# Performance work log

Hardware: AMD Instinct MI355X
Metric: run time of the kernel (lower is better)

The kernel has to match this reference:

```python
import jax, jax.numpy as jnp
import numpy as np

N_NODES = 100000
N_EDGES = 1600000
NIN = 128
NHID = 128
N_GRAPHS = 1024


def _gcn_conv(x, src, dst, norm, W, b, n_nodes):
    """PyG-style GCNConv: linear (no bias) -> normalized scatter-add -> + bias."""
    xw = x @ W                                   # [N, out]
    msg = xw[src] * norm[:, None]                # gather + edge-normalize, [E', out]
    out = jax.ops.segment_sum(msg, dst, num_segments=n_nodes)
    return out + b


def _gcn_norm(edge_index, n_nodes):
    """Add self-loops and compute symmetric deg^{-1/2} normalization per edge."""
    loops = jnp.arange(n_nodes, dtype=edge_index.dtype)
    src = jnp.concatenate([edge_index[0], loops])
    dst = jnp.concatenate([edge_index[1], loops])
    deg = jax.ops.segment_sum(jnp.ones_like(dst, dtype=jnp.float32), dst,
                              num_segments=n_nodes)
    deg_isqrt = jnp.where(deg > 0, jax.lax.rsqrt(jnp.maximum(deg, 1.0)), 0.0)
    norm = deg_isqrt[src] * deg_isqrt[dst]
    return src, dst, norm


def setup_inputs() -> dict:
    key = jax.random.key(0)
    ks = jax.random.split(key, 8)
    x = jax.random.normal(ks[0], (N_NODES, NIN), dtype=jnp.float32)
    edge_index = jax.random.randint(ks[1], (2, N_EDGES), 0, N_NODES, dtype=jnp.int64)
    batch = jnp.sort(jax.random.randint(ks[2], (N_NODES,), 0, N_GRAPHS, dtype=jnp.int64))
    s_in = 1.0 / np.sqrt(NIN)
    s_h = 1.0 / np.sqrt(NHID)
    return {
        "x": x,
        "edge_index": edge_index,
        "batch": batch,
        "W1": jax.random.normal(ks[3], (NIN, NHID), dtype=jnp.float32) * s_in,
        "b1": jnp.zeros((NHID,), dtype=jnp.float32),
        "W2": jax.random.normal(ks[4], (NHID, NHID), dtype=jnp.float32) * s_h,
        "b2": jnp.zeros((NHID,), dtype=jnp.float32),
        "W3": jax.random.normal(ks[5], (NHID, NHID), dtype=jnp.float32) * s_h,
        "b3": jnp.zeros((NHID,), dtype=jnp.float32),
        "Wfc": jax.random.normal(ks[6], (NHID, 1), dtype=jnp.float32) * s_h,
        "bfc": jnp.zeros((1,), dtype=jnp.float32),
    }


def reference(x, edge_index, batch, W1, b1, W2, b2, W3, b3, Wfc, bfc):
    n_nodes = x.shape[0]
    src, dst, norm = _gcn_norm(edge_index, n_nodes)
    h = jax.nn.relu(_gcn_conv(x, src, dst, norm, W1, b1, n_nodes))
    h = jax.nn.relu(_gcn_conv(h, src, dst, norm, W2, b2, n_nodes))
    h = jax.nn.relu(_gcn_conv(h, src, dst, norm, W3, b3, n_nodes))
    # global mean pool over graphs in the batch
    sums = jax.ops.segment_sum(h, batch, num_segments=N_GRAPHS)      # [G, NHID]
    cnts = jax.ops.segment_sum(jnp.ones((n_nodes,), dtype=h.dtype), batch,
                               num_segments=N_GRAPHS)
    pooled = sums / jnp.maximum(cnts, 1.0)[:, None]
    return pooled @ Wfc + bfc                                        # [G, 1]
```

## Files before the change

### kernel.cpp

```cpp
#include <hip/hip_runtime.h>

#define N_NODES   100000
#define N_EDGES   1600000
#define NFEAT     128
#define N_GRAPHS  1024

#define BSHIFT  6
#define NBUCK   1563
#define NSUB    8
#define SUBCAP  256
#define CURSTRIDE 16

typedef unsigned int uint32;
typedef unsigned short ushort;
typedef __attribute__((ext_vector_type(8))) short short8;
typedef __attribute__((ext_vector_type(4))) float f32x4;

__device__ inline ushort f2b(float f) {
    uint32 x = __float_as_uint(f);
    uint32 r = x + 0x7fffu + ((x >> 16) & 1u);
    return (ushort)(r >> 16);
}
__device__ inline float blo(uint32 u) { return __uint_as_float(u << 16); }
__device__ inline float bhi(uint32 u) { return __uint_as_float(u & 0xffff0000u); }

__global__ __launch_bounds__(256) void k_scatter(const int* __restrict__ src, const int* __restrict__ dst,
                                                 int* __restrict__ cur, uint32* __restrict__ bbuf) {
    int e = blockIdx.x * 256 + threadIdx.x;
    int sub = blockIdx.x & (NSUB - 1);
    if (e < N_EDGES) {
        int s = src[e], d = dst[e];
        int b = d >> BSHIFT;
        int slot = (b << 3) | sub;
        int p = atomicAdd(&cur[slot * CURSTRIDE], 1);
        if (p < SUBCAP)
            bbuf[slot * SUBCAP + p] = (uint32)(((d & 63) << 17) | s);
    }
}

__global__ __launch_bounds__(256) void k_bucketscan(const int* __restrict__ cur, int* __restrict__ bucketBase,
                                                    int* __restrict__ offsets) {
    __shared__ int wsum[4];
    int t = threadIdx.x;
    int v[7];
    int ts = 0;
    #pragma unroll
    for (int i = 0; i < 7; ++i) {
        int b = t * 7 + i;
        int sz = 0;
        if (b < NBUCK) {
            #pragma unroll
            for (int s = 0; s < NSUB; ++s) {
                int c = cur[((b << 3) | s) * CURSTRIDE];
                sz += (c < SUBCAP) ? c : SUBCAP;
            }
        }
        v[i] = sz;
        ts += sz;
    }
    int lane = t & 63, w = t >> 6;
    int inc = ts;
    #pragma unroll
    for (int d = 1; d < 64; d <<= 1) {
        int u = __shfl_up(inc, d, 64);
        if (lane >= d) inc += u;
    }
    if (lane == 63) wsum[w] = inc;
    __syncthreads();
    int wpre = 0;
    for (int i = 0; i < w; ++i) wpre += wsum[i];
    int run = wpre + inc - ts;
    #pragma unroll
    for (int i = 0; i < 7; ++i) {
        int b = t * 7 + i;
        if (b < NBUCK) bucketBase[b] = run;
        run += v[i];
    }
    if (t == 255) offsets[N_NODES] = run;
}

__global__ __launch_bounds__(256) void k_build(const uint32* __restrict__ bbuf, const int* __restrict__ cur,
                                               const int* __restrict__ bucketBase, int* __restrict__ col,
                                               int* __restrict__ offsets, float* __restrict__ dinv) {
    int b = blockIdx.x;
    __shared__ uint32 ebuf[NSUB * SUBCAP];
    __shared__ int sorted[NSUB * SUBCAP];
    __shared__ int hist[64], lcur[64];
    __shared__ int subOff[NSUB + 1];
    int t = threadIdx.x;
    if (t == 0) {
        int run = 0;
        #pragma unroll
        for (int s = 0; s < NSUB; ++s) {
            subOff[s] = run;
            int c = cur[((b << 3) | s) * CURSTRIDE];
            run += (c < SUBCAP) ? c : SUBCAP;
        }
        subOff[NSUB] = run;
    }
    if (t < 64) hist[t] = 0;
    __syncthreads();
    int cnt = subOff[NSUB];
    #pragma unroll
    for (int s = 0; s < NSUB; ++s) {
        int n = subOff[s + 1] - subOff[s];
        const uint32* p = bbuf + ((b << 3) | s) * SUBCAP;
        for (int i = t; i < n; i += 256) ebuf[subOff[s] + i] = p[i];
    }
    __syncthreads();
    for (int i = t; i < cnt; i += 256) atomicAdd(&hist[ebuf[i] >> 17], 1);
    __syncthreads();
    int nb = b << BSHIFT;
    if (t < 64) {
        int c = hist[t];
        int inc = c;
        #pragma unroll
        for (int d = 1; d < 64; d <<= 1) {
            int u = __shfl_up(inc, d, 64);
            if (t >= d) inc += u;
        }
        int excl = inc - c;
        lcur[t] = excl;
        int node = nb + t;
        if (node < N_NODES) {
            offsets[node] = bucketBase[b] + excl;
            dinv[node] = rsqrtf((float)(c + 1));
        }
    }
    __syncthreads();
    for (int i = t; i < cnt; i += 256) {
        uint32 p = ebuf[i];
        int lp = atomicAdd(&lcur[p >> 17], 1);
        sorted[lp] = (int)(p & 0x1FFFF);
    }
    __syncthreads();
    int base = bucketBase[b];
    for (int i = t; i < cnt; i += 256) col[base + i] = sorted[i];
}

__global__ __launch_bounds__(256) void k_castw(const float* __restrict__ W1, const float* __restrict__ W2,
                                               const float* __restrict__ W3, ushort* __restrict__ WT) {
    int i = blockIdx.x * blockDim.x + threadIdx.x;
    if (i >= 3 * NFEAT * NFEAT) return;
    int l = i >> 14;
    int j = i & 16383;
    int n = j >> 7;
    int k = j & 127;
    const float* W = (l == 0) ? W1 : (l == 1) ? W2 : W3;
    WT[i] = f2b(W[k * NFEAT + n]);
}

#define WT_STRIDE 136
#define GEMM_EPILOGUE \
    __syncthreads(); \
    { \
        ushort* sC = sWT; \
        int colBase = lane & 15; \
        _Pragma("unroll") \
        for (int r = 0; r < 4; ++r) { \
            int lr = wave * 16 + kg * 4 + r; \
            _Pragma("unroll") \
            for (int nt = 0; nt < 8; ++nt) \
                sC[lr * NFEAT + nt * 16 + colBase] = f2b(acc[nt][r]); \
        } \
    } \
    __syncthreads(); \
    { \
        int rowBase = blockIdx.x * 64; \
        const float4* sC4 = (const float4*)sWT; \
        for (int i = t; i < 1024; i += 256) { \
            int row = i >> 4; \
            int gr = rowBase + row; \
            if (gr < M) ((float4*)(C + (size_t)gr * NFEAT))[i & 15] = sC4[i]; \
        } \
    }

__global__ __launch_bounds__(256) void k_gemm(const ushort* __restrict__ A,
                                              const ushort* __restrict__ WTl,
                                              ushort* __restrict__ C, int M) {
    __shared__ ushort sWT[NFEAT * WT_STRIDE];
    int t = threadIdx.x;
    for (int i = t; i < NFEAT * 16; i += 256) {
        int n = i >> 4, c = i & 15;
        *(float4*)(sWT + n * WT_STRIDE + c * 8) = ((const float4*)WTl)[i];
    }
    int wave = t >> 6, lane = t & 63;
    int m0 = blockIdx.x * 64 + wave * 16;
    int mRow = m0 + (lane & 15);
    if (mRow >= M) mRow = M - 1;
    int kg = lane >> 4;
    const short8* Ap = (const short8*)(A + (size_t)mRow * NFEAT + kg * 8);
    short8 a0 = Ap[0];
    short8 a1 = Ap[4];
    short8 a2 = Ap[8];
    short8 a3 = Ap[12];
    __syncthreads();

    f32x4 acc[8];
    #pragma unroll
    for (int nt = 0; nt < 8; ++nt) acc[nt] = (f32x4){0.f, 0.f, 0.f, 0.f};

    #pragma unroll
    for (int nt = 0; nt < 8; ++nt) {
        int n = nt * 16 + (lane & 15);
        const short8* Bp = (const short8*)(sWT + n * WT_STRIDE + kg * 8);
        short8 b0 = Bp[0];
        short8 b1 = Bp[4];
        short8 b2 = Bp[8];
        short8 b3 = Bp[12];
        acc[nt] = __builtin_amdgcn_mfma_f32_16x16x32_bf16(a0, b0, acc[nt], 0, 0, 0);
        acc[nt] = __builtin_amdgcn_mfma_f32_16x16x32_bf16(a1, b1, acc[nt], 0, 0, 0);
        acc[nt] = __builtin_amdgcn_mfma_f32_16x16x32_bf16(a2, b2, acc[nt], 0, 0, 0);
        acc[nt] = __builtin_amdgcn_mfma_f32_16x16x32_bf16(a3, b3, acc[nt], 0, 0, 0);
    }
    GEMM_EPILOGUE
}

__device__ inline short8 cvt8(const float* p) {
    float4 v0 = ((const float4*)p)[0];
    float4 v1 = ((const float4*)p)[1];
    short8 r;
    r[0] = (short)f2b(v0.x); r[1] = (short)f2b(v0.y);
    r[2] = (short)f2b(v0.z); r[3] = (short)f2b(v0.w);
    r[4] = (short)f2b(v1.x); r[5] = (short)f2b(v1.y);
    r[6] = (short)f2b(v1.z); r[7] = (short)f2b(v1.w);
    return r;
}

__global__ __launch_bounds__(256) void k_gemm_x(const float* __restrict__ A,
                                                const ushort* __restrict__ WTl,
                                                ushort* __restrict__ C, int M) {
    __shared__ ushort sWT[NFEAT * WT_STRIDE];
    int t = threadIdx.x;
    for (int i = t; i < NFEAT * 16; i += 256) {
        int n = i >> 4, c = i & 15;
        *(float4*)(sWT + n * WT_STRIDE + c * 8) = ((const float4*)WTl)[i];
    }
    int wave = t >> 6, lane = t & 63;
    int m0 = blockIdx.x * 64 + wave * 16;
    int mRow = m0 + (lane & 15);
    if (mRow >= M) mRow = M - 1;
    int kg = lane >> 4;
    const float* Ap = A + (size_t)mRow * NFEAT + kg * 8;
    short8 a0 = cvt8(Ap);
    short8 a1 = cvt8(Ap + 32);
    short8 a2 = cvt8(Ap + 64);
    short8 a3 = cvt8(Ap + 96);
    __syncthreads();

    f32x4 acc[8];
    #pragma unroll
    for (int nt = 0; nt < 8; ++nt) acc[nt] = (f32x4){0.f, 0.f, 0.f, 0.f};

    #pragma unroll
    for (int nt = 0; nt < 8; ++nt) {
        int n = nt * 16 + (lane & 15);
        const short8* Bp = (const short8*)(sWT + n * WT_STRIDE + kg * 8);
        short8 b0 = Bp[0];
        short8 b1 = Bp[4];
        short8 b2 = Bp[8];
        short8 b3 = Bp[12];
        acc[nt] = __builtin_amdgcn_mfma_f32_16x16x32_bf16(a0, b0, acc[nt], 0, 0, 0);
        acc[nt] = __builtin_amdgcn_mfma_f32_16x16x32_bf16(a1, b1, acc[nt], 0, 0, 0);
        acc[nt] = __builtin_amdgcn_mfma_f32_16x16x32_bf16(a2, b2, acc[nt], 0, 0, 0);
        acc[nt] = __builtin_amdgcn_mfma_f32_16x16x32_bf16(a3, b3, acc[nt], 0, 0, 0);
    }
    GEMM_EPILOGUE
}

#define AGG_BODY4 \
    float dn = dinv[n]; \
    int half = lane >> 4; \
    int fl = lane & 15; \
    const uint4* XW4 = (const uint4*)XWu; \
    uint4 sv = XW4[(size_t)n * 16 + fl]; \
    float ws = (half == 0) ? dn * dn : 0.f; \
    float a0 = ws * blo(sv.x), a1 = ws * bhi(sv.x); \
    float a2 = ws * blo(sv.y), a3 = ws * bhi(sv.y); \
    float a4 = ws * blo(sv.z), a5 = ws * bhi(sv.z); \
    float a6 = ws * blo(sv.w), a7 = ws * bhi(sv.w); \
    int e0 = off[n], e1 = off[n + 1]; \
    for (int base = e0; base < e1; base += 64) { \
        int len = e1 - base; if (len > 64) len = 64; \
        int cm = (lane < len) ? col[base + lane] : 0; \
        float wm = (lane < len) ? dn * dinv[cm] : 0.f; \
        int j = 0; \
        for (; j + 16 <= len; j += 16) { \
            uint4 u[4]; float w[4]; \
            _Pragma("unroll") \
            for (int p = 0; p < 4; ++p) { \
                int idx = j + 4 * p + half; \
                int cc = __shfl(cm, idx, 64); \
                w[p] = __shfl(wm, idx, 64); \
                u[p] = XW4[(size_t)cc * 16 + fl]; \
            } \
            _Pragma("unroll") \
            for (int p = 0; p < 4; ++p) { \
                a0 = fmaf(w[p], blo(u[p].x), a0); a1 = fmaf(w[p], bhi(u[p].x), a1); \
                a2 = fmaf(w[p], blo(u[p].y), a2); a3 = fmaf(w[p], bhi(u[p].y), a3); \
                a4 = fmaf(w[p], blo(u[p].z), a4); a5 = fmaf(w[p], bhi(u[p].z), a5); \
                a6 = fmaf(w[p], blo(u[p].w), a6); a7 = fmaf(w[p], bhi(u[p].w), a7); \
            } \
        } \
        for (; j < len; j += 4) { \
            int rem = len - j; \
            int idx = j + ((half < rem) ? half : 0); \
            int cc = __shfl(cm, idx, 64); \
            float ww = __shfl(wm, idx, 64); \
            if (half >= rem) ww = 0.f; \
            uint4 u = XW4[(size_t)cc * 16 + fl]; \
            a0 = fmaf(ww, blo(u.x), a0); a1 = fmaf(ww, bhi(u.x), a1); \
            a2 = fmaf(ww, blo(u.y), a2); a3 = fmaf(ww, bhi(u.y), a3); \
            a4 = fmaf(ww, blo(u.z), a4); a5 = fmaf(ww, bhi(u.z), a5); \
            a6 = fmaf(ww, blo(u.w), a6); a7 = fmaf(ww, bhi(u.w), a7); \
        } \
    } \
    a0 += __shfl_xor(a0, 32, 64); a0 += __shfl_xor(a0, 16, 64); \
    a1 += __shfl_xor(a1, 32, 64); a1 += __shfl_xor(a1, 16, 64); \
    a2 += __shfl_xor(a2, 32, 64); a2 += __shfl_xor(a2, 16, 64); \
    a3 += __shfl_xor(a3, 32, 64); a3 += __shfl_xor(a3, 16, 64); \
    a4 += __shfl_xor(a4, 32, 64); a4 += __shfl_xor(a4, 16, 64); \
    a5 += __shfl_xor(a5, 32, 64); a5 += __shfl_xor(a5, 16, 64); \
    a6 += __shfl_xor(a6, 32, 64); a6 += __shfl_xor(a6, 16, 64); \
    a7 += __shfl_xor(a7, 32, 64); a7 += __shfl_xor(a7, 16, 64);

__global__ __launch_bounds__(256) void k_agg(const uint32* __restrict__ XWu, const int* __restrict__ col,
                                             const int* __restrict__ off, const float* __restrict__ dinv,
                                             const float* __restrict__ bias, uint32* __restrict__ Hu) {
    int wid = (blockIdx.x * blockDim.x + threadIdx.x) >> 6;
    int lane = threadIdx.x & 63;
    if (wid >= N_NODES) return;
    int n = wid;
    AGG_BODY4
    if (half == 0) {
        float4 bb0 = ((const float4*)bias)[2 * fl];
        float4 bb1 = ((const float4*)bias)[2 * fl + 1];
        float r0 = fmaxf(a0 + bb0.x, 0.f), r1 = fmaxf(a1 + bb0.y, 0.f);
        float r2 = fmaxf(a2 + bb0.z, 0.f), r3 = fmaxf(a3 + bb0.w, 0.f);
        float r4 = fmaxf(a4 + bb1.x, 0.f), r5 = fmaxf(a5 + bb1.y, 0.f);
        float r6 = fmaxf(a6 + bb1.z, 0.f), r7 = fmaxf(a7 + bb1.w, 0.f);
        uint4 o;
        o.x = (uint32)f2b(r0) | ((uint32)f2b(r1) << 16);
        o.y = (uint32)f2b(r2) | ((uint32)f2b(r3) << 16);
        o.z = (uint32)f2b(r4) | ((uint32)f2b(r5) << 16);
        o.w = (uint32)f2b(r6) | ((uint32)f2b(r7) << 16);
        ((uint4*)Hu)[(size_t)n * 16 + fl] = o;
    }
}

__global__ __launch_bounds__(256) void k_agg_fc(const uint32* __restrict__ XWu, const int* __restrict__ col,
                                                const int* __restrict__ off, const float* __restrict__ dinv,
                                                const float* __restrict__ bias, const float* __restrict__ Wfc,
                                                float* __restrict__ nodeS) {
    int wid = (blockIdx.x * blockDim.x + threadIdx.x) >> 6;
    int lane = threadIdx.x & 63;
    if (wid >= N_NODES) return;
    int n = wid;
    AGG_BODY4
    float4 bb0 = ((const float4*)bias)[2 * fl];
    float4 bb1 = ((const float4*)bias)[2 * fl + 1];
    float4 wf0 = ((const float4*)Wfc)[2 * fl];
    float4 wf1 = ((const float4*)Wfc)[2 * fl + 1];
    float s = fmaxf(a0 + bb0.x, 0.f) * wf0.x + fmaxf(a1 + bb0.y, 0.f) * wf0.y
            + fmaxf(a2 + bb0.z, 0.f) * wf0.z + fmaxf(a3 + bb0.w, 0.f) * wf0.w
            + fmaxf(a4 + bb1.x, 0.f) * wf1.x + fmaxf(a5 + bb1.y, 0.f) * wf1.y
            + fmaxf(a6 + bb1.z, 0.f) * wf1.z + fmaxf(a7 + bb1.w, 0.f) * wf1.w;
    s += __shfl_xor(s, 8, 64);
    s += __shfl_xor(s, 4, 64);
    s += __shfl_xor(s, 2, 64);
    s += __shfl_xor(s, 1, 64);
    if (lane == 0) nodeS[n] = s;
}

__device__ inline int lower_bound_dev(const int* a, int n, int key) {
    int lo = 0, hi = n;
    while (lo < hi) {
        int mid = (lo + hi) >> 1;
        if (a[mid] < key) lo = mid + 1; else hi = mid;
    }
    return lo;
}

__global__ __launch_bounds__(256) void k_pool(const float* __restrict__ nodeS, const int* __restrict__ batch,
                                              const float* __restrict__ bfc, float* __restrict__ out) {
    int g = blockIdx.x;
    int t = threadIdx.x;
    int lo = lower_bound_dev(batch, N_NODES, g);
    int hi = lower_bound_dev(batch, N_NODES, g + 1);
    float s = 0.f;
    for (int i = lo + t; i < hi; i += 256) s += nodeS[i];
    for (int d = 32; d > 0; d >>= 1) s += __shfl_down(s, d, 64);
    __shared__ float ws[4];
    int lane = t & 63, w = t >> 6;
    if (lane == 0) ws[w] = s;
    __syncthreads();
    if (t == 0) {
        float tot = ws[0] + ws[1] + ws[2] + ws[3];
        float cnt = (float)(hi - lo);
        out[g] = tot / fmaxf(cnt, 1.0f) + bfc[0];
    }
}

extern "C" void kernel_launch(void* const* d_in, const int* in_sizes, int n_in,
                              void* d_out, int out_size, void* d_ws, size_t ws_size,
                              hipStream_t stream) {
    const float* x    = (const float*)d_in[0];
    const int*   ei   = (const int*)d_in[1];
    const int*   batch= (const int*)d_in[2];
    const float* W1   = (const float*)d_in[3];
    const float* b1   = (const float*)d_in[4];
    const float* W2   = (const float*)d_in[5];
    const float* b2   = (const float*)d_in[6];
    const float* W3   = (const float*)d_in[7];
    const float* b3   = (const float*)d_in[8];
    const float* Wfc  = (const float*)d_in[9];
    const float* bfc  = (const float*)d_in[10];
    float* out = (float*)d_out;

    const int* src = ei;
    const int* dst = ei + N_EDGES;

    char* p = (char*)d_ws;
    auto carve = [&](size_t bytes) { void* r = (void*)p; p += (bytes + 255) & ~(size_t)255; return r; };
    int*    cur       = (int*)   carve(sizeof(int) * (size_t)NBUCK * NSUB * CURSTRIDE);
    uint32* bbuf      = (uint32*)carve(sizeof(uint32) * (size_t)NBUCK * NSUB * SUBCAP);
    int*    bucketBase= (int*)   carve(sizeof(int) * (NBUCK + 1));
    float*  dinv      = (float*) carve(sizeof(float) * N_NODES);
    int*    offsets   = (int*)   carve(sizeof(int) * (N_NODES + 1));
    int*    col       = (int*)   carve(sizeof(int) * N_EDGES);
    ushort* XW        = (ushort*)carve(sizeof(short) * (size_t)N_NODES * NFEAT);
    ushort* H         = (ushort*)carve(sizeof(short) * (size_t)N_NODES * NFEAT);
    ushort* WT        = (ushort*)carve(sizeof(short) * 3 * NFEAT * NFEAT);
    float*  nodeS     = (float*) carve(sizeof(float) * N_NODES);

    const int edgeBlocks = (N_EDGES + 255) / 256;
    const int waveNodeBlocks = (N_NODES * 64 + 255) / 256;
    const int gemmBlocks = (N_NODES + 63) / 64;

    hipMemsetAsync(cur, 0, sizeof(int) * (size_t)NBUCK * NSUB * CURSTRIDE, stream);
    k_scatter<<<edgeBlocks, 256, 0, stream>>>(src, dst, cur, bbuf);
    k_bucketscan<<<1, 256, 0, stream>>>(cur, bucketBase, offsets);
    k_build<<<NBUCK, 256, 0, stream>>>(bbuf, cur, bucketBase, col, offsets, dinv);

    k_castw<<<(3 * NFEAT * NFEAT + 255) / 256, 256, 0, stream>>>(W1, W2, W3, WT);

    k_gemm_x<<<gemmBlocks, 256, 0, stream>>>(x, WT, XW, N_NODES);
    k_agg<<<waveNodeBlocks, 256, 0, stream>>>((const uint32*)XW, col, offsets, dinv, b1, (uint32*)H);
    k_gemm<<<gemmBlocks, 256, 0, stream>>>(H, WT + NFEAT * NFEAT, XW, N_NODES);
    k_agg<<<waveNodeBlocks, 256, 0, stream>>>((const uint32*)XW, col, offsets, dinv, b2, (uint32*)H);
    k_gemm<<<gemmBlocks, 256, 0, stream>>>(H, WT + 2 * NFEAT * NFEAT, XW, N_NODES);
    k_agg_fc<<<waveNodeBlocks, 256, 0, stream>>>((const uint32*)XW, col, offsets, dinv, b3, Wfc, nodeS);

    k_pool<<<N_GRAPHS, 256, 0, stream>>>(nodeS, batch, bfc, out);
}
```

Baseline: 433.6 us.

## Replace per-edge global atomics with block-local binning in CSR build scatter

New measurement: 393.2 us. -9.3%, faster.

```diff
diff --git a/kernel.cpp b/kernel.cpp
--- a/kernel.cpp
+++ b/kernel.cpp
@@ -5,11 +5,12 @@
 #define NFEAT     128
 #define N_GRAPHS  1024
 
-#define BSHIFT  6
-#define NBUCK   1563
-#define NSUB    8
-#define SUBCAP  256
-#define CURSTRIDE 16
+#define BSHIFT  8
+#define BNODES  256
+#define NBUCK   391
+#define BCAP    4608
+#define SC_EDGES 8192
+#define SC_BLOCKS 196
 
 typedef unsigned int uint32;
 typedef unsigned short ushort;
@@ -26,15 +27,62 @@
 
 __global__ __launch_bounds__(256) void k_scatter(const int* __restrict__ src, const int* __restrict__ dst,
                                                  int* __restrict__ cur, uint32* __restrict__ bbuf) {
-    int e = blockIdx.x * 256 + threadIdx.x;
-    int sub = blockIdx.x & (NSUB - 1);
-    if (e < N_EDGES) {
-        int s = src[e], d = dst[e];
+    __shared__ int hist[NBUCK];
+    __shared__ int lofs[NBUCK];
+    __shared__ int lcur[NBUCK];
+    __shared__ int gbase[NBUCK];
+    __shared__ int wsum[4];
+    __shared__ uint32 sortedP[SC_EDGES];
+    __shared__ ushort sortedB[SC_EDGES];
+    int t = threadIdx.x;
+    int e0 = blockIdx.x * SC_EDGES;
+    int total = N_EDGES - e0; if (total > SC_EDGES) total = SC_EDGES; if (total < 0) total = 0;
+
+    for (int i = t; i < NBUCK; i += 256) hist[i] = 0;
+    __syncthreads();
+    for (int i = t; i < total; i += 256)
+        atomicAdd(&hist[dst[e0 + i] >> BSHIFT], 1);
+    __syncthreads();
+    {
+        int b0 = 2 * t, b1 = 2 * t + 1;
+        int h0 = (b0 < NBUCK) ? hist[b0] : 0;
+        int h1 = (b1 < NBUCK) ? hist[b1] : 0;
+        int ts = h0 + h1;
+        int lane = t & 63, w = t >> 6;
+        int inc = ts;
+        #pragma unroll
+        for (int d = 1; d < 64; d <<= 1) {
+            int u = __shfl_up(inc, d, 64);
+            if (lane >= d) inc += u;
+        }
+        if (lane == 63) wsum[w] = inc;
+        __syncthreads();
+        int wpre = 0;
+        for (int i = 0; i < w; ++i) wpre += wsum[i];
+        int run = wpre + inc - ts;
+        if (b0 < NBUCK) {
+            lofs[b0] = run; lcur[b0] = run;
+            if (h0) gbase[b0] = atomicAdd(&cur[b0], h0);
+        }
+        if (b1 < NBUCK) {
+            lofs[b1] = run + h0; lcur[b1] = run + h0;
+            if (h1) gbase[b1] = atomicAdd(&cur[b1], h1);
+        }
+    }
+    __syncthreads();
+    for (int i = t; i < total; i += 256) {
+        int s = src[e0 + i], d = dst[e0 + i];
         int b = d >> BSHIFT;
-        int slot = (b << 3) | sub;
-        int p = atomicAdd(&cur[slot * CURSTRIDE], 1);
-        if (p < SUBCAP)
-            bbuf[slot * SUBCAP + p] = (uint32)(((d & 63) << 17) | s);
+        int p = atomicAdd(&lcur[b], 1);
+        sortedP[p] = ((uint32)(d & (BNODES - 1)) << 17) | (uint32)s;
+        sortedB[p] = (ushort)b;
+    }
+    __syncthreads();
+    for (int i = t; i < total; i += 256) {
+        int b = sortedB[i];
+        int addr = gbase[b] + (i - lofs[b]);
+        if (addr < BCAP)
+            bbuf[(size_t)b * BCAP + addr] = sortedP[i];
     }
 }
 
@@ -42,22 +90,11 @@
                                                     int* __restrict__ offsets) {
     __shared__ int wsum[4];
     int t = threadIdx.x;
-    int v[7];
-    int ts = 0;
-    #pragma unroll
-    for (int i = 0; i < 7; ++i) {
-        int b = t * 7 + i;
-        int sz = 0;
-        if (b < NBUCK) {
-            #pragma unroll
-            for (int s = 0; s < NSUB; ++s) {
-                int c = cur[((b << 3) | s) * CURSTRIDE];
-                sz += (c < SUBCAP) ? c : SUBCAP;
-            }
-        }
-        v[i] = sz;
-        ts += sz;
-    }
+    int b0 = 2 * t, b1 = 2 * t + 1;
+    int h0 = 0, h1 = 0;
+    if (b0 < NBUCK) { h0 = cur[b0]; if (h0 > BCAP) h0 = BCAP; }
+    if (b1 < NBUCK) { h1 = cur[b1]; if (h1 > BCAP) h1 = BCAP; }
+    int ts = h0 + h1;
     int lane = t & 63, w = t >> 6;
     int inc = ts;
     #pragma unroll
@@ -70,58 +107,41 @@
     int wpre = 0;
     for (int i = 0; i < w; ++i) wpre += wsum[i];
     int run = wpre + inc - ts;
-    #pragma unroll
-    for (int i = 0; i < 7; ++i) {
-        int b = t * 7 + i;
-        if (b < NBUCK) bucketBase[b] = run;
-        run += v[i];
-    }
-    if (t == 255) offsets[N_NODES] = run;
+    if (b0 < NBUCK) bucketBase[b0] = run;
+    if (b1 < NBUCK) bucketBase[b1] = run + h0;
+    if (t == 255) offsets[N_NODES] = run + ts;
 }
 
 __global__ __launch_bounds__(256) void k_build(const uint32* __restrict__ bbuf, const int* __restrict__ cur,
                                                const int* __restrict__ bucketBase, int* __restrict__ col,
                                                int* __restrict__ offsets, float* __restrict__ dinv) {
     int b = blockIdx.x;
-    __shared__ uint32 ebuf[NSUB * SUBCAP];
-    __shared__ int sorted[NSUB * SUBCAP];
-    __shared__ int hist[64], lcur[64];
-    __shared__ int subOff[NSUB + 1];
-    int t = threadIdx.x;
-    if (t == 0) {
-        int run = 0;
-        #pragma unroll
-        for (int s = 0; s < NSUB; ++s) {
-            subOff[s] = run;
-            int c = cur[((b << 3) | s) * CURSTRIDE];
-            run += (c < SUBCAP) ? c : SUBCAP;
-        }
-        subOff[NSUB] = run;
-    }
-    if (t < 64) hist[t] = 0;
-    __syncthreads();
-    int cnt = subOff[NSUB];
-    #pragma unroll
-    for (int s = 0; s < NSUB; ++s) {
-        int n = subOff[s + 1] - subOff[s];
-        const uint32* p = bbuf + ((b << 3) | s) * SUBCAP;
-        for (int i = t; i < n; i += 256) ebuf[subOff[s] + i] = p[i];
-    }
-    __syncthreads();
-    for (int i = t; i < cnt; i += 256) atomicAdd(&hist[ebuf[i] >> 17], 1);
-    __syncthreads();
-    int nb = b << BSHIFT;
-    if (t < 64) {
+    __shared__ int hist[BNODES], lcur[BNODES];
+    __shared__ int wsum[4];
+    __shared__ int sorted[BCAP];
+    int t = threadIdx.x;
+    int cnt = cur[b]; if (cnt > BCAP) cnt = BCAP;
+    const uint32* reg = bbuf + (size_t)b * BCAP;
+    hist[t] = 0;
+    __syncthreads();
+    for (int i = t; i < cnt; i += 256) atomicAdd(&hist[reg[i] >> 17], 1);
+    __syncthreads();
+    {
         int c = hist[t];
+        int lane = t & 63, w = t >> 6;
         int inc = c;
         #pragma unroll
         for (int d = 1; d < 64; d <<= 1) {
             int u = __shfl_up(inc, d, 64);
-            if (t >= d) inc += u;
+            if (lane >= d) inc += u;
         }
-        int excl = inc - c;
+        if (lane == 63) wsum[w] = inc;
+        __syncthreads();
+        int wpre = 0;
+        for (int i = 0; i < w; ++i) wpre += wsum[i];
+        int excl = wpre + inc - c;
         lcur[t] = excl;
-        int node = nb + t;
+        int node = (b << BSHIFT) + t;
         if (node < N_NODES) {
             offsets[node] = bucketBase[b] + excl;
             dinv[node] = rsqrtf((float)(c + 1));
@@ -129,7 +149,7 @@
     }
     __syncthreads();
     for (int i = t; i < cnt; i += 256) {
-        uint32 p = ebuf[i];
+        uint32 p = reg[i];
         int lp = atomicAdd(&lcur[p >> 17], 1);
         sorted[lp] = (int)(p & 0x1FFFF);
     }
@@ -422,8 +442,8 @@
 
     char* p = (char*)d_ws;
     auto carve = [&](size_t bytes) { void* r = (void*)p; p += (bytes + 255) & ~(size_t)255; return r; };
-    int*    cur       = (int*)   carve(sizeof(int) * (size_t)NBUCK * NSUB * CURSTRIDE);
-    uint32* bbuf      = (uint32*)carve(sizeof(uint32) * (size_t)NBUCK * NSUB * SUBCAP);
+    int*    cur       = (int*)   carve(sizeof(int) * NBUCK);
+    uint32* bbuf      = (uint32*)carve(sizeof(uint32) * (size_t)NBUCK * BCAP);
     int*    bucketBase= (int*)   carve(sizeof(int) * (NBUCK + 1));
     float*  dinv      = (float*) carve(sizeof(float) * N_NODES);
     int*    offsets   = (int*)   carve(sizeof(int) * (N_NODES + 1));
@@ -433,12 +453,11 @@
     ushort* WT        = (ushort*)carve(sizeof(short) * 3 * NFEAT * NFEAT);
     float*  nodeS     = (float*) carve(sizeof(float) * N_NODES);
 
-    const int edgeBlocks = (N_EDGES + 255) / 256;
     const int waveNodeBlocks = (N_NODES * 64 + 255) / 256;
     const int gemmBlocks = (N_NODES + 63) / 64;
 
-    hipMemsetAsync(cur, 0, sizeof(int) * (size_t)NBUCK * NSUB * CURSTRIDE, stream);
-    k_scatter<<<edgeBlocks, 256, 0, stream>>>(src, dst, cur, bbuf);
+    hipMemsetAsync(cur, 0, sizeof(int) * NBUCK, stream);
+    k_scatter<<<SC_BLOCKS, 256, 0, stream>>>(src, dst, cur, bbuf);
     k_bucketscan<<<1, 256, 0, stream>>>(cur, bucketBase, offsets);
     k_build<<<NBUCK, 256, 0, stream>>>(bbuf, cur, bucketBase, col, offsets, dinv);
 
```
